# Optimization experiments

Measured on AMD Instinct MI355X. Metric: run time of the kernel, lower is better.

## Reference

```python
import jax, jax.numpy as jnp
import numpy as np

B, N, D = 4, 4096, 512
K = 16384          # codebook size
NUM_Q = 2          # residual quantizers (shared codebook)


def setup_inputs() -> dict:
    key = jax.random.key(0)
    ks = jax.random.split(key, 6)
    s = 1.0 / np.sqrt(D)
    return {
        "x": jax.random.normal(ks[0], (B, N, D), dtype=jnp.float32),
        "enc_w": jax.random.normal(ks[1], (D, D), dtype=jnp.float32) * s,
        "enc_b": jnp.zeros((D,), dtype=jnp.float32),
        "codebook": jax.random.normal(ks[2], (K, D), dtype=jnp.float32),
        "dec_w": jax.random.normal(ks[3], (D, D), dtype=jnp.float32) * s,
        "dec_b": jnp.zeros((D,), dtype=jnp.float32),
    }


def _residual_vq(z, codebook):
    # z: [B, N, D] -> flatten tokens
    flat = z.reshape(-1, z.shape[-1])          # [T, D]
    c_sq = jnp.sum(codebook * codebook, axis=-1)  # [K]
    q_sum = jnp.zeros_like(flat)
    residual = flat
    for _ in range(NUM_Q):
        # argmin of ||r - c||^2 == argmin of (||c||^2 - 2 r.c); skip ||r||^2
        dists = c_sq[None, :] - 2.0 * (residual @ codebook.T)  # [T, K]
        idx = jnp.argmin(dists, axis=-1)                       # [T]
        q = codebook[idx]                                      # gather [T, D]
        q_sum = q_sum + q
        residual = residual - q
    return q_sum.reshape(z.shape)


def reference(x, enc_w, enc_b, codebook, dec_w, dec_b):
    z = x @ enc_w.T + enc_b                     # encoder Linear(512 -> 512)
    q = _residual_vq(z, codebook)               # sum of per-stage code vectors
    z_tilde = z + jax.lax.stop_gradient(q - z)  # straight-through estimator
    x_recon = z_tilde @ dec_w.T + dec_b         # decoder Linear(512 -> 512)
    return x_recon
```

## Files before the change

kernel.cpp:

```cpp
#include <hip/hip_runtime.h>
#include <stdint.h>

constexpr int TT = 16384;
constexpr int DD = 512;
constexpr int KK = 16384;
constexpr int TOPK = 8;

typedef __bf16 bf16x8 __attribute__((ext_vector_type(8)));
typedef __bf16 bf16x4 __attribute__((ext_vector_type(4)));
typedef float f32x4 __attribute__((ext_vector_type(4)));

typedef const __attribute__((address_space(1))) void* gas_ptr;
typedef __attribute__((address_space(3))) void* las_ptr;

__device__ __forceinline__ unsigned long long pack_di(float d, int idx) {
    uint32_t u = __float_as_uint(d);
    u = (u & 0x80000000u) ? ~u : (u | 0x80000000u);
    return ((unsigned long long)u << 32) | (uint32_t)idx;
}

__device__ __forceinline__ unsigned long long umin64(unsigned long long a,
                                                     unsigned long long b) {
    return a < b ? a : b;
}
__device__ __forceinline__ uint32_t umin32(uint32_t a, uint32_t b) { return a < b ? a : b; }
__device__ __forceinline__ uint32_t umax32(uint32_t a, uint32_t b) { return a > b ? a : b; }

__device__ __forceinline__ uint32_t sortable(float d) {
    uint32_t u = __float_as_uint(d);
    return u ^ ((uint32_t)((int32_t)u >> 31) | 0x80000000u);
}

template<int MODE>
__global__ __launch_bounds__(256)
void gemm_mfma(const float* __restrict__ A, const float* __restrict__ A2,
               const float* __restrict__ W, const float* __restrict__ bias,
               float* __restrict__ out0, float* __restrict__ out1,
               __bf16* __restrict__ out2)
{
    __shared__ __bf16 Ah[128 * 64], Al[128 * 64];
    __shared__ __bf16 Bh[128 * 64], Bl[128 * 64];
    const int tid = threadIdx.x;
    const int lane = tid & 63;
    const int w = tid >> 6;
    const int row0 = blockIdx.y * 128;
    const int col0 = blockIdx.x * 128;

    f32x4 acc[2][8] = {};

    const int sr = tid >> 4;
    const int scol = (tid & 15) * 4;
    const int lcol = (((scol >> 3) ^ (sr & 7)) << 3) + (scol & 7);

    int a_off[2], b_off[8];
    #pragma unroll
    for (int mi = 0; mi < 2; ++mi) {
        const int ar = w * 32 + mi * 16 + (lane & 15);
        a_off[mi] = ar * 64 + (((lane >> 4) ^ (ar & 7)) << 3);
    }
    #pragma unroll
    for (int ni = 0; ni < 8; ++ni) {
        const int br = ni * 16 + (lane & 15);
        b_off[ni] = br * 64 + (((lane >> 4) ^ (br & 7)) << 3);
    }

    for (int kb = 0; kb < 512; kb += 64) {
        __syncthreads();
        #pragma unroll
        for (int i = 0; i < 8; ++i) {
            const int r = i * 16 + sr;
            float4 v = *(const float4*)(A + (size_t)(row0 + r) * 512 + kb + scol);
            if (MODE == 1) {
                const float4 u = *(const float4*)(A2 + (size_t)(row0 + r) * 512 + kb + scol);
                v.x -= u.x; v.y -= u.y; v.z -= u.z; v.w -= u.w;
            }
            bf16x4 hv, lv;
            hv[0] = (__bf16)v.x; hv[1] = (__bf16)v.y; hv[2] = (__bf16)v.z; hv[3] = (__bf16)v.w;
            lv[0] = (__bf16)(v.x - (float)hv[0]); lv[1] = (__bf16)(v.y - (float)hv[1]);
            lv[2] = (__bf16)(v.z - (float)hv[2]); lv[3] = (__bf16)(v.w - (float)hv[3]);
            *(bf16x4*)(Ah + r * 64 + lcol) = hv;
            *(bf16x4*)(Al + r * 64 + lcol) = lv;

            const float4 x = *(const float4*)(W + (size_t)(col0 + r) * 512 + kb + scol);
            bf16x4 hw, lw;
            hw[0] = (__bf16)x.x; hw[1] = (__bf16)x.y; hw[2] = (__bf16)x.z; hw[3] = (__bf16)x.w;
            lw[0] = (__bf16)(x.x - (float)hw[0]); lw[1] = (__bf16)(x.y - (float)hw[1]);
            lw[2] = (__bf16)(x.z - (float)hw[2]); lw[3] = (__bf16)(x.w - (float)hw[3]);
            *(bf16x4*)(Bh + r * 64 + lcol) = hw;
            *(bf16x4*)(Bl + r * 64 + lcol) = lw;
        }
        __syncthreads();
        #pragma unroll
        for (int s = 0; s < 2; ++s) {
            const int sx = s * 32;
            bf16x8 ah[2], al[2];
            #pragma unroll
            for (int mi = 0; mi < 2; ++mi) {
                ah[mi] = *(const bf16x8*)(Ah + (a_off[mi] ^ sx));
                al[mi] = *(const bf16x8*)(Al + (a_off[mi] ^ sx));
            }
            #pragma unroll
            for (int ni = 0; ni < 8; ++ni) {
                const bf16x8 bh = *(const bf16x8*)(Bh + (b_off[ni] ^ sx));
                const bf16x8 bl = *(const bf16x8*)(Bl + (b_off[ni] ^ sx));
                #pragma unroll
                for (int mi = 0; mi < 2; ++mi) {
                    acc[mi][ni] = __builtin_amdgcn_mfma_f32_16x16x32_bf16(ah[mi], bh, acc[mi][ni], 0, 0, 0);
                    acc[mi][ni] = __builtin_amdgcn_mfma_f32_16x16x32_bf16(ah[mi], bl, acc[mi][ni], 0, 0, 0);
                    acc[mi][ni] = __builtin_amdgcn_mfma_f32_16x16x32_bf16(al[mi], bh, acc[mi][ni], 0, 0, 0);
                }
            }
        }
    }

    #pragma unroll
    for (int mi = 0; mi < 2; ++mi) {
        #pragma unroll
        for (int reg = 0; reg < 4; ++reg) {
            const int row = row0 + w * 32 + mi * 16 + (lane >> 4) * 4 + reg;
            #pragma unroll
            for (int ni = 0; ni < 8; ++ni) {
                const int col = col0 + ni * 16 + (lane & 15);
                const float o = acc[mi][ni][reg] + bias[col];
                out0[(size_t)row * 512 + col] = o;
                if (MODE == 0) {
                    out1[(size_t)row * 512 + col] = o;
                    out2[(size_t)row * 512 + col] = (__bf16)o;
                }
            }
        }
    }
}

__global__ __launch_bounds__(256)
void dist_approx(const __bf16* __restrict__ Rh,
                 const __bf16* __restrict__ Ch,
                 const float* __restrict__ csq,
                 uint32_t* __restrict__ winners)
{
    __shared__ __bf16 As[128 * 32];
    __shared__ __bf16 Bs[128 * 32];
    const int tid = threadIdx.x;
    const int lane = tid & 63;
    const int w = tid >> 6;
    const int wm = w >> 1, wn = w & 1;
    const int row0 = blockIdx.y * 128;
    const int col0 = blockIdx.x * 128;

    f32x4 acc[4][4] = {};

    const int srow0 = w * 32 + (lane >> 2);
    const int srow1 = srow0 + 16;
    const int gc0 = (lane & 3) ^ ((srow0 >> 1) & 3);
    const int gc1 = (lane & 3) ^ ((srow1 >> 1) & 3);
    __bf16* ldsA0 = As + (w * 32 + 0) * 32;
    __bf16* ldsA1 = As + (w * 32 + 16) * 32;
    __bf16* ldsB0 = Bs + (w * 32 + 0) * 32;
    __bf16* ldsB1 = Bs + (w * 32 + 16) * 32;

    int a_off[4], b_off[4];
    #pragma unroll
    for (int i = 0; i < 4; ++i) {
        const int ar = wm * 64 + i * 16 + (lane & 15);
        a_off[i] = ar * 32 + (((lane >> 4) ^ ((ar >> 1) & 3)) << 3);
        const int br = wn * 64 + i * 16 + (lane & 15);
        b_off[i] = br * 32 + (((lane >> 4) ^ ((br >> 1) & 3)) << 3);
    }

    for (int kb = 0; kb < 512; kb += 32) {
        __syncthreads();
        __builtin_amdgcn_global_load_lds(
            (gas_ptr)(Rh + (size_t)(row0 + srow0) * 512 + kb + gc0 * 8), (las_ptr)ldsA0, 16, 0, 0);
        __builtin_amdgcn_global_load_lds(
            (gas_ptr)(Rh + (size_t)(row0 + srow1) * 512 + kb + gc1 * 8), (las_ptr)ldsA1, 16, 0, 0);
        __builtin_amdgcn_global_load_lds(
            (gas_ptr)(Ch + (size_t)(col0 + srow0) * 512 + kb + gc0 * 8), (las_ptr)ldsB0, 16, 0, 0);
        __builtin_amdgcn_global_load_lds(
            (gas_ptr)(Ch + (size_t)(col0 + srow1) * 512 + kb + gc1 * 8), (las_ptr)ldsB1, 16, 0, 0);
        __syncthreads();

        bf16x8 af[4], bfr[4];
        #pragma unroll
        for (int i = 0; i < 4; ++i) af[i]  = *(const bf16x8*)(As + a_off[i]);
        #pragma unroll
        for (int i = 0; i < 4; ++i) bfr[i] = *(const bf16x8*)(Bs + b_off[i]);
        #pragma unroll
        for (int mi = 0; mi < 4; ++mi)
            #pragma unroll
            for (int ni = 0; ni < 4; ++ni)
                acc[mi][ni] = __builtin_amdgcn_mfma_f32_16x16x32_bf16(
                    af[mi], bfr[ni], acc[mi][ni], 0, 0, 0);
    }

    float csv[4];
    #pragma unroll
    for (int ni = 0; ni < 4; ++ni)
        csv[ni] = csq[col0 + wn * 64 + ni * 16 + (lane & 15)];

    const int tile = blockIdx.x * 2 + wn;
    #pragma unroll
    for (int mi = 0; mi < 4; ++mi) {
        #pragma unroll
        for (int reg = 0; reg < 4; ++reg) {
            uint32_t b = 0xFFFFFFFFu, s = 0xFFFFFFFFu;
            #pragma unroll
            for (int ni = 0; ni < 4; ++ni) {
                const float d = fmaf(-2.0f, acc[mi][ni][reg], csv[ni]);
                const uint32_t key = (sortable(d) & 0xFFFFFFC0u)
                                   | (uint32_t)(ni * 16 + (lane & 15));
                const uint32_t nb = umin32(b, key);
                s = umin32(s, umax32(b, key));
                b = nb;
            }
            #pragma unroll
            for (int m = 1; m < 16; m <<= 1) {
                const uint32_t ob = __shfl_xor((int)b, m, 16);
                const uint32_t os = __shfl_xor((int)s, m, 16);
                const uint32_t nb = umin32(b, ob);
                s = umin32(umin32(s, os), umax32(b, ob));
                b = nb;
            }
            if ((lane & 15) == 0) {
                const int row = row0 + wm * 64 + mi * 16 + (lane >> 4) * 4 + reg;
                uint2 v; v.x = b; v.y = s;
                *(uint2*)(winners + (size_t)row * 512 + tile * 2) = v;
            }
        }
    }
}

__global__ __launch_bounds__(256)
void select_rescore(const uint32_t* __restrict__ winners,
                    const float* __restrict__ CB, const float* __restrict__ csq,
                    float* __restrict__ R, __bf16* __restrict__ R16)
{
    const int w = threadIdx.x >> 6;
    const int lane = threadIdx.x & 63;
    const int token = blockIdx.x * 4 + w;

    const uint32_t* wt = winners + (size_t)token * 512;
    uint4 q0 = *(const uint4*)(wt + lane * 8);
    uint4 q1 = *(const uint4*)(wt + lane * 8 + 4);
    uint32_t k32[8] = {q0.x, q0.y, q0.z, q0.w, q1.x, q1.y, q1.z, q1.w};

    unsigned long long v[8];
    #pragma unroll
    for (int j = 0; j < 8; ++j) {
        const int gcol = ((lane * 8 + j) >> 1) * 64 + (int)(k32[j] & 63u);
        v[j] = ((unsigned long long)k32[j] << 32) | (uint32_t)gcol;
    }

    unsigned long long cand[TOPK];
    #pragma unroll
    for (int t = 0; t < TOPK; ++t) {
        unsigned long long mm = v[0];
        #pragma unroll
        for (int j = 1; j < 8; ++j) mm = umin64(mm, v[j]);
        #pragma unroll
        for (int m = 1; m < 64; m <<= 1)
            mm = umin64(mm, __shfl_xor(mm, m, 64));
        cand[t] = mm;
        #pragma unroll
        for (int j = 0; j < 8; ++j) if (v[j] == mm) v[j] = ~0ull;
    }

    float4 r0 = *(const float4*)(R + (size_t)token * 512 + lane * 8);
    float4 r1 = *(const float4*)(R + (size_t)token * 512 + lane * 8 + 4);

    unsigned long long best = ~0ull;
    #pragma unroll
    for (int t = 0; t < TOPK; ++t) {
        const int col = (int)(cand[t] & 0xFFFFFFFFull);
        const float4 c0 = *(const float4*)(CB + (size_t)col * 512 + lane * 8);
        const float4 c1 = *(const float4*)(CB + (size_t)col * 512 + lane * 8 + 4);
        float dot = r0.x * c0.x;
        dot = fmaf(r0.y, c0.y, dot); dot = fmaf(r0.z, c0.z, dot);
        dot = fmaf(r0.w, c0.w, dot); dot = fmaf(r1.x, c1.x, dot);
        dot = fmaf(r1.y, c1.y, dot); dot = fmaf(r1.z, c1.z, dot);
        dot = fmaf(r1.w, c1.w, dot);
        #pragma unroll
        for (int m = 1; m < 64; m <<= 1) dot += __shfl_xor(dot, m, 64);
        const float d = fmaf(-2.0f, dot, csq[col]);
        best = umin64(best, pack_di(d, col));
    }

    const int bcol = (int)(best & 0xFFFFFFFFull);
    const float4 c0 = *(const float4*)(CB + (size_t)bcol * 512 + lane * 8);
    const float4 c1 = *(const float4*)(CB + (size_t)bcol * 512 + lane * 8 + 4);
    r0.x -= c0.x; r0.y -= c0.y; r0.z -= c0.z; r0.w -= c0.w;
    r1.x -= c1.x; r1.y -= c1.y; r1.z -= c1.z; r1.w -= c1.w;
    *(float4*)(R + (size_t)token * 512 + lane * 8) = r0;
    *(float4*)(R + (size_t)token * 512 + lane * 8 + 4) = r1;
    bf16x8 h;
    h[0] = (__bf16)r0.x; h[1] = (__bf16)r0.y; h[2] = (__bf16)r0.z; h[3] = (__bf16)r0.w;
    h[4] = (__bf16)r1.x; h[5] = (__bf16)r1.y; h[6] = (__bf16)r1.z; h[7] = (__bf16)r1.w;
    *(bf16x8*)(R16 + (size_t)token * 512 + lane * 8) = h;
}

__global__ __launch_bounds__(256)
void prep_cb(const float* __restrict__ CB, float* __restrict__ c_sq,
             __bf16* __restrict__ cb16)
{
    const int wave = threadIdx.x >> 6;
    const int lane = threadIdx.x & 63;
    const int row = blockIdx.x * 4 + wave;
    const float* p = CB + (size_t)row * DD + lane * 8;
    const float4 a = *(const float4*)p;
    const float4 b = *(const float4*)(p + 4);
    bf16x8 h;
    h[0] = (__bf16)a.x; h[1] = (__bf16)a.y; h[2] = (__bf16)a.z; h[3] = (__bf16)a.w;
    h[4] = (__bf16)b.x; h[5] = (__bf16)b.y; h[6] = (__bf16)b.z; h[7] = (__bf16)b.w;
    *(bf16x8*)(cb16 + (size_t)row * DD + lane * 8) = h;
    float s = a.x*a.x + a.y*a.y + a.z*a.z + a.w*a.w
            + b.x*b.x + b.y*b.y + b.z*b.z + b.w*b.w;
    #pragma unroll
    for (int m = 1; m < 64; m <<= 1) s += __shfl_xor(s, m, 64);
    if (lane == 0) c_sq[row] = s;
}

extern "C" void kernel_launch(void* const* d_in, const int* in_sizes, int n_in,
                              void* d_out, int out_size, void* d_ws, size_t ws_size,
                              hipStream_t stream)
{
    const float* x    = (const float*)d_in[0];
    const float* encw = (const float*)d_in[1];
    const float* encb = (const float*)d_in[2];
    const float* cb   = (const float*)d_in[3];
    const float* decw = (const float*)d_in[4];
    const float* decb = (const float*)d_in[5];
    float* out = (float*)d_out;

    float* z    = (float*)d_ws;
    float* r    = z + (size_t)TT * DD;
    __bf16* cb16 = (__bf16*)(r + (size_t)TT * DD);
    __bf16* r16  = cb16 + (size_t)KK * DD;
    float* csq  = (float*)(r16 + (size_t)TT * DD);
    uint32_t* winners = (uint32_t*)d_out;

    const dim3 blk(256);

    gemm_mfma<0><<<dim3(DD / 128, TT / 128), blk, 0, stream>>>(
        x, nullptr, encw, encb, z, r, r16);

    prep_cb<<<dim3(KK / 4), blk, 0, stream>>>(cb, csq, cb16);

    for (int s = 0; s < 2; ++s) {
        dist_approx<<<dim3(KK / 128, TT / 128), blk, 0, stream>>>(r16, cb16, csq, winners);
        select_rescore<<<dim3(TT / 4), blk, 0, stream>>>(winners, cb, csq, r, r16);
    }

    gemm_mfma<1><<<dim3(DD / 128, TT / 128), blk, 0, stream>>>(
        z, r, decw, decb, out, nullptr, nullptr);
}
```

Measured before the change: 1.107 ms.

## Rewrite distance GEMM as 256x256 tiled, double-buffered, 8-wave pipelined kernel

Replaces the 128x128 single-buffered distance GEMM with a 256x256 tile kernel using 512 threads, a 64-wide K step, and double-buffered LDS. Global-to-LDS loads for the next K slice are interleaved with MFMA phases, paced by barriers, explicit vmcnt/lgkmcnt waits and s_setprio. Workgroups are remapped across XCDs for codebook/token locality. The larger tile cuts global traffic per FLOP and hides load latency, at the cost of heavy LDS use (128KB per block) and more registers, which may limit occupancy.

```diff
diff --git a/kernel.cpp b/kernel.cpp
--- a/kernel.cpp
+++ b/kernel.cpp
@@ -132,64 +132,145 @@
     }
 }
 
-__global__ __launch_bounds__(256)
-void dist_approx(const __bf16* __restrict__ Rh,
-                 const __bf16* __restrict__ Ch,
-                 const float* __restrict__ csq,
-                 uint32_t* __restrict__ winners)
+__global__ __launch_bounds__(512, 2)
+void dist_approx8(const __bf16* __restrict__ Rh,
+                  const __bf16* __restrict__ Ch,
+                  const float* __restrict__ csq,
+                  uint32_t* __restrict__ winners)
 {
-    __shared__ __bf16 As[128 * 32];
-    __shared__ __bf16 Bs[128 * 32];
-    const int tid = threadIdx.x;
+    __shared__ __bf16 As[2][256 * 64];
+    __shared__ __bf16 Bs[2][256 * 64];
+
+    const int tid  = threadIdx.x;
     const int lane = tid & 63;
-    const int w = tid >> 6;
-    const int wm = w >> 1, wn = w & 1;
-    const int row0 = blockIdx.y * 128;
-    const int col0 = blockIdx.x * 128;
-
-    f32x4 acc[4][4] = {};
-
-    const int srow0 = w * 32 + (lane >> 2);
-    const int srow1 = srow0 + 16;
-    const int gc0 = (lane & 3) ^ ((srow0 >> 1) & 3);
-    const int gc1 = (lane & 3) ^ ((srow1 >> 1) & 3);
-    __bf16* ldsA0 = As + (w * 32 + 0) * 32;
-    __bf16* ldsA1 = As + (w * 32 + 16) * 32;
-    __bf16* ldsB0 = Bs + (w * 32 + 0) * 32;
-    __bf16* ldsB1 = Bs + (w * 32 + 16) * 32;
-
-    int a_off[4], b_off[4];
-    #pragma unroll
-    for (int i = 0; i < 4; ++i) {
-        const int ar = wm * 64 + i * 16 + (lane & 15);
-        a_off[i] = ar * 32 + (((lane >> 4) ^ ((ar >> 1) & 3)) << 3);
-        const int br = wn * 64 + i * 16 + (lane & 15);
-        b_off[i] = br * 32 + (((lane >> 4) ^ ((br >> 1) & 3)) << 3);
-    }
-
-    for (int kb = 0; kb < 512; kb += 32) {
-        __syncthreads();
-        __builtin_amdgcn_global_load_lds(
-            (gas_ptr)(Rh + (size_t)(row0 + srow0) * 512 + kb + gc0 * 8), (las_ptr)ldsA0, 16, 0, 0);
-        __builtin_amdgcn_global_load_lds(
-            (gas_ptr)(Rh + (size_t)(row0 + srow1) * 512 + kb + gc1 * 8), (las_ptr)ldsA1, 16, 0, 0);
-        __builtin_amdgcn_global_load_lds(
-            (gas_ptr)(Ch + (size_t)(col0 + srow0) * 512 + kb + gc0 * 8), (las_ptr)ldsB0, 16, 0, 0);
-        __builtin_amdgcn_global_load_lds(
-            (gas_ptr)(Ch + (size_t)(col0 + srow1) * 512 + kb + gc1 * 8), (las_ptr)ldsB1, 16, 0, 0);
-        __syncthreads();
-
-        bf16x8 af[4], bfr[4];
-        #pragma unroll
-        for (int i = 0; i < 4; ++i) af[i]  = *(const bf16x8*)(As + a_off[i]);
-        #pragma unroll
-        for (int i = 0; i < 4; ++i) bfr[i] = *(const bf16x8*)(Bs + b_off[i]);
-        #pragma unroll
-        for (int mi = 0; mi < 4; ++mi)
-            #pragma unroll
-            for (int ni = 0; ni < 4; ++ni)
-                acc[mi][ni] = __builtin_amdgcn_mfma_f32_16x16x32_bf16(
-                    af[mi], bfr[ni], acc[mi][ni], 0, 0, 0);
+    const int w    = tid >> 6;
+    const int wm   = w >> 2;
+    const int wn   = w & 3;
+
+    const int wg   = (blockIdx.x & 7) * 512 + (blockIdx.x >> 3);
+    const int col0 = (wg & 63) << 8;
+    const int row0 = (wg >> 6) << 8;
+
+    f32x4 acc[8][4] = {};
+
+    const int s_r = tid >> 3;
+    const int s_c = (tid & 7) ^ (s_r & 7);
+    const __bf16* aS = Rh + (size_t)(row0 + s_r) * 512 + s_c * 8;
+    const __bf16* bS = Ch + (size_t)(col0 + s_r) * 512 + s_c * 8;
+    __bf16* const lA0 = &As[0][0]; __bf16* const lA1 = &As[1][0];
+    __bf16* const lB0 = &Bs[0][0]; __bf16* const lB1 = &Bs[1][0];
+
+#define STAGE(SRC, UOFF, DST)                                                      \
+    {                                                                              \
+        __builtin_amdgcn_global_load_lds((gas_ptr)((SRC) + (UOFF)),                \
+                                         (las_ptr)((DST) + w * 8 * 64), 16, 0, 0); \
+        __builtin_amdgcn_global_load_lds((gas_ptr)((SRC) + (UOFF) + 64 * 512),     \
+                                         (las_ptr)((DST) + (64 + w * 8) * 64), 16, 0, 0); \
+    }
+
+    int aoff[8], boff[4];
+    #pragma unroll
+    for (int mi = 0; mi < 8; ++mi) {
+        const int r = wm * 128 + mi * 16 + (lane & 15);
+        aoff[mi] = r * 64 + (((lane >> 4) ^ (r & 7)) << 3);
+    }
+    #pragma unroll
+    for (int ni = 0; ni < 4; ++ni) {
+        const int r = wn * 64 + ni * 16 + (lane & 15);
+        boff[ni] = r * 64 + (((lane >> 4) ^ (r & 7)) << 3);
+    }
+
+#define BAR __builtin_amdgcn_s_barrier()
+#define LGKM0 { asm volatile("s_waitcnt lgkmcnt(0)" ::: "memory"); \
+                __builtin_amdgcn_sched_barrier(0); }
+#define MFMA_QUAD(AF, A0, BV)                                                  \
+    {                                                                          \
+        __builtin_amdgcn_s_setprio(1);                                         \
+        _Pragma("unroll")                                                      \
+        for (int mi = 0; mi < 4; ++mi) {                                       \
+            _Pragma("unroll")                                                  \
+            for (int ni = 0; ni < 4; ++ni)                                     \
+                acc[(A0) + mi][ni] = __builtin_amdgcn_mfma_f32_16x16x32_bf16(  \
+                    (AF)[(A0) + mi], (BV)[ni], acc[(A0) + mi][ni], 0, 0, 0);   \
+        }                                                                      \
+        __builtin_amdgcn_s_setprio(0);                                         \
+    }
+
+    STAGE(aS, 0,              lA0);
+    STAGE(aS, 128 * 512,      lA0 + 128 * 64);
+    STAGE(bS, 0,              lB0);
+    STAGE(bS, 128 * 512,      lB0 + 128 * 64);
+    STAGE(aS, 64,             lA1);
+    STAGE(aS, 128 * 512 + 64, lA1 + 128 * 64);
+    asm volatile("s_waitcnt vmcnt(4)" ::: "memory");
+    BAR;
+
+    bf16x8 a0[8], a1[8], b0[4], b1[4];
+
+    for (int it = 0; it < 4; ++it) {
+        const bool more = it < 3;
+        const int kb1 = (2 * it + 1) * 64;
+        const int kb2 = (2 * it + 2) * 64;
+        const int kb3 = (2 * it + 3) * 64;
+
+        #pragma unroll
+        for (int mi = 0; mi < 8; ++mi) a0[mi] = *(const bf16x8*)(lA0 + aoff[mi]);
+        #pragma unroll
+        for (int ni = 0; ni < 4; ++ni) b0[ni] = *(const bf16x8*)(lB0 + boff[ni]);
+        STAGE(bS, kb1, lB1);
+        BAR; LGKM0;
+        MFMA_QUAD(a0, 0, b0);
+        BAR;
+
+        #pragma unroll
+        for (int mi = 0; mi < 8; ++mi) a1[mi] = *(const bf16x8*)(lA0 + (aoff[mi] ^ 32));
+        STAGE(bS, 128 * 512 + kb1, lB1 + 128 * 64);
+        BAR; LGKM0;
+        MFMA_QUAD(a0, 4, b0);
+        BAR;
+
+        #pragma unroll
+        for (int ni = 0; ni < 4; ++ni) b1[ni] = *(const bf16x8*)(lB0 + (boff[ni] ^ 32));
+        if (more) STAGE(aS, kb2, lA0);
+        BAR; LGKM0;
+        MFMA_QUAD(a1, 0, b1);
+        BAR;
+
+        if (more) STAGE(aS, 128 * 512 + kb2, lA0 + 128 * 64);
+        BAR;
+        MFMA_QUAD(a1, 4, b1);
+        if (more) { asm volatile("s_waitcnt vmcnt(4)" ::: "memory"); }
+        else      { asm volatile("s_waitcnt vmcnt(0)" ::: "memory"); }
+        BAR;
+
+        #pragma unroll
+        for (int mi = 0; mi < 8; ++mi) a0[mi] = *(const bf16x8*)(lA1 + aoff[mi]);
+        #pragma unroll
+        for (int ni = 0; ni < 4; ++ni) b0[ni] = *(const bf16x8*)(lB1 + boff[ni]);
+        if (more) STAGE(bS, kb2, lB0);
+        BAR; LGKM0;
+        MFMA_QUAD(a0, 0, b0);
+        BAR;
+
+        #pragma unroll
+        for (int mi = 0; mi < 8; ++mi) a1[mi] = *(const bf16x8*)(lA1 + (aoff[mi] ^ 32));
+        if (more) STAGE(bS, 128 * 512 + kb2, lB0 + 128 * 64);
+        BAR; LGKM0;
+        MFMA_QUAD(a0, 4, b0);
+        BAR;
+
+        #pragma unroll
+        for (int ni = 0; ni < 4; ++ni) b1[ni] = *(const bf16x8*)(lB1 + (boff[ni] ^ 32));
+        if (more) STAGE(aS, kb3, lA1);
+        BAR; LGKM0;
+        MFMA_QUAD(a1, 0, b1);
+        BAR;
+
+        if (more) STAGE(aS, 128 * 512 + kb3, lA1 + 128 * 64);
+        BAR;
+        MFMA_QUAD(a1, 4, b1);
+        if (more) { asm volatile("s_waitcnt vmcnt(4)" ::: "memory"); }
+        BAR;
     }
 
     float csv[4];
@@ -197,9 +278,9 @@
     for (int ni = 0; ni < 4; ++ni)
         csv[ni] = csq[col0 + wn * 64 + ni * 16 + (lane & 15)];
 
-    const int tile = blockIdx.x * 2 + wn;
-    #pragma unroll
-    for (int mi = 0; mi < 4; ++mi) {
+    const int tile = (col0 >> 6) + wn;
+    #pragma unroll
+    for (int mi = 0; mi < 8; ++mi) {
         #pragma unroll
         for (int reg = 0; reg < 4; ++reg) {
             uint32_t b = 0xFFFFFFFFu, s = 0xFFFFFFFFu;
@@ -221,12 +302,16 @@
                 b = nb;
             }
             if ((lane & 15) == 0) {
-                const int row = row0 + wm * 64 + mi * 16 + (lane >> 4) * 4 + reg;
+                const int row = row0 + wm * 128 + mi * 16 + (lane >> 4) * 4 + reg;
                 uint2 v; v.x = b; v.y = s;
                 *(uint2*)(winners + (size_t)row * 512 + tile * 2) = v;
             }
         }
     }
+#undef STAGE
+#undef BAR
+#undef LGKM0
+#undef MFMA_QUAD
 }
 
 __global__ __launch_bounds__(256)
@@ -345,7 +430,8 @@
     prep_cb<<<dim3(KK / 4), blk, 0, stream>>>(cb, csq, cb16);
 
     for (int s = 0; s < 2; ++s) {
-        dist_approx<<<dim3(KK / 128, TT / 128), blk, 0, stream>>>(r16, cb16, csq, winners);
+        dist_approx8<<<dim3((TT / 256) * (KK / 256)), dim3(512), 0, stream>>>(
+            r16, cb16, csq, winners);
         select_rescore<<<dim3(TT / 4), blk, 0, stream>>>(winners, cb, csq, r, r16);
     }
 
```

Measured after the change: 1.129 ms. 1.02x slower.
